# Kernel optimization log

Hardware: AMD Instinct MI355X
Metric: run time of the kernel (lower is better)

The kernel has to match this reference:

```python
import jax, jax.numpy as jnp
import numpy as np

EPS = 1e-5  # BatchNorm eps (torch default)


def setup_inputs() -> dict:
    key = jax.random.key(0)
    ks = jax.random.split(key, 12)
    C, Ci, B, H, W = 64, 32, 2, 96, 96  # plane, inter_plane=plane//2

    def n(k, shape, s=0.05):
        return jax.random.normal(k, shape, jnp.float32) * s

    return {
        "xA": jax.random.normal(ks[0], (B, C, H, W), jnp.float32),
        "xB": jax.random.normal(ks[1], (B, C, H, W), jnp.float32),
        "Wk": n(ks[2], (Ci, C)), "bk": n(ks[3], (Ci,)),
        "Wv": n(ks[4], (Ci, C)), "bv": n(ks[5], (Ci,)),
        "Wq": n(ks[6], (Ci, C)), "bq": n(ks[7], (Ci,)),
        "Wg": n(ks[8], (Ci, Ci)),  # conv_wg, 1x1 Conv1d, no bias
        "g1_gamma": jnp.ones((Ci,), jnp.float32), "g1_beta": jnp.zeros((Ci,), jnp.float32),
        "g1_mean": jnp.zeros((Ci,), jnp.float32), "g1_var": jnp.ones((Ci,), jnp.float32),
        "Wo": n(ks[9], (C, Ci)), "bo": n(ks[10], (C,)),
        "g2_gamma": jnp.ones((C,), jnp.float32), "g2_beta": jnp.zeros((C,), jnp.float32),
        "g2_mean": jnp.zeros((C,), jnp.float32), "g2_var": jnp.ones((C,), jnp.float32),
    }


def reference(xA, xB, Wk, bk, Wv, bv, Wq, bq, Wg,
              g1_gamma, g1_beta, g1_mean, g1_var,
              Wo, bo, g2_gamma, g2_beta, g2_mean, g2_var):
    B, C, H, W = xB.shape
    N = H * W
    # 1x1 conv2d projections -> [B, Ci, N]
    k = (jnp.einsum('bchw,oc->bohw', xA, Wk) + bk[None, :, None, None]).reshape(B, -1, N)
    v = (jnp.einsum('bchw,oc->bohw', xA, Wv) + bv[None, :, None, None]).reshape(B, -1, N)
    q = (jnp.einsum('bchw,oc->bohw', xB, Wq) + bq[None, :, None, None]).reshape(B, -1, N)
    # AV = softmax(v^T @ q, axis=2)  -> [B, N, N]
    A = jax.nn.softmax(jnp.einsum('bcn,bcm->bnm', v, q), axis=2)
    # k @ AV -> [B, Ci, N]
    av = jnp.einsum('bcn,bnm->bcm', k, A)
    # conv_wg (1x1 conv1d, no bias) + BatchNorm1d (inference form)
    av = jnp.einsum('oc,bcn->bon', Wg, av)
    av = (av - g1_mean[None, :, None]) * (g1_gamma / jnp.sqrt(g1_var + EPS))[None, :, None] + g1_beta[None, :, None]
    av = av.reshape(B, -1, H, W)
    # out: 1x1 conv2d -> plane, BatchNorm2d, residual, relu
    o = jnp.einsum('oc,bchw->bohw', Wo, av) + bo[None, :, None, None]
    o = (o - g2_mean[None, :, None, None]) * (g2_gamma / jnp.sqrt(g2_var + EPS))[None, :, None, None] + g2_beta[None, :, None, None]
    return jax.nn.relu(o + xB)
```

## Files before the change

### kernel.cpp

```cpp
#include <hip/hip_runtime.h>
#include <hip/hip_bf16.h>

#define CI 32
#define CC 64
#define NBATCH 2
#define NPIX 9216
#define NSD 24
#define LOG2E 1.4426950408889634f

typedef __attribute__((ext_vector_type(8))) short s16x8;
typedef __attribute__((ext_vector_type(4))) short s16x4;
typedef __attribute__((ext_vector_type(4))) float f32x4;
typedef __attribute__((ext_vector_type(2))) unsigned int u32x2;
typedef __attribute__((ext_vector_type(4))) unsigned int u32x4;

static __device__ __forceinline__ unsigned cvtpk(float a, float b) {
    unsigned d;
    asm("v_cvt_pk_bf16_f32 %0, %1, %2" : "=v"(d) : "v"(a), "v"(b));
    return d;
}
static __device__ __forceinline__ short f2b(float f) {
    union { float f; unsigned u; } v; v.f = f;
    return (short)((v.u + 0x7FFFu + ((v.u >> 16) & 1u)) >> 16);
}
static __device__ __forceinline__ float b2f(short s) {
    union { unsigned u; float f; } v; v.u = ((unsigned)(unsigned short)s) << 16;
    return v.f;
}

__global__ __launch_bounds__(256) void k_proj(
    const float* __restrict__ xA, const float* __restrict__ xB,
    const float* __restrict__ Wk, const float* __restrict__ bk,
    const float* __restrict__ Wv, const float* __restrict__ bv,
    const float* __restrict__ Wq, const float* __restrict__ bq,
    short* __restrict__ vT, short* __restrict__ qT, short* __restrict__ kC)
{
    int mode = blockIdx.y;
    const float* W    = mode == 0 ? Wk : (mode == 1 ? Wv : Wq);
    const float* bias = mode == 0 ? bk : (mode == 1 ? bv : bq);
    const float* X    = mode == 2 ? xB : xA;

    __shared__ float sW[CI * CC];
    __shared__ float sb[CI];
    __shared__ float spart[3][64][33];
    for (int i = threadIdx.x; i < CI * CC; i += 256) sW[i] = W[i];
    if (threadIdx.x < CI) sb[threadIdx.x] = bias[threadIdx.x];
    __syncthreads();

    int q4 = threadIdx.x >> 6;
    int lp = threadIdx.x & 63;
    int idx = blockIdx.x * 64 + lp;
    int b = idx / NPIX, n = idx % NPIX;

    float acc[CI];
    #pragma unroll
    for (int o = 0; o < CI; o++) acc[o] = 0.f;

    const float* px = X + (size_t)b * CC * NPIX + n;
    #pragma unroll
    for (int cc = 0; cc < 16; cc++) {
        int c = q4 * 16 + cc;
        float x = px[(size_t)c * NPIX];
        #pragma unroll
        for (int o = 0; o < CI; o++) acc[o] += sW[o * CC + c] * x;
    }
    if (q4) {
        #pragma unroll
        for (int o = 0; o < CI; o++) spart[q4 - 1][lp][o] = acc[o];
    }
    __syncthreads();
    if (q4 == 0) {
        #pragma unroll
        for (int o = 0; o < CI; o++)
            acc[o] += spart[0][lp][o] + spart[1][lp][o] + spart[2][lp][o] + sb[o];
        if (mode == 0) {
            #pragma unroll
            for (int o = 0; o < CI; o++)
                kC[((size_t)b * CI + o) * NPIX + n] = f2b(acc[o]);
        } else {
            float sc = (mode == 2) ? LOG2E : 1.0f;
            short* dst = (mode == 1 ? vT : qT) + ((size_t)b * NPIX + n) * CI;
            #pragma unroll
            for (int v4 = 0; v4 < 4; v4++) {
                u32x4 pk;
                #pragma unroll
                for (int j = 0; j < 4; j++)
                    pk[j] = cvtpk(acc[v4 * 8 + 2 * j] * sc, acc[v4 * 8 + 2 * j + 1] * sc);
                ((u32x4*)dst)[v4] = pk;
            }
        }
    }
}

__global__ __launch_bounds__(128) void k_denom(
    const short* __restrict__ vT, const short* __restrict__ qT,
    float* __restrict__ sum_part)
{
    int w = threadIdx.x >> 6, lane = threadIdx.x & 63;
    int r = lane & 15, g = lane >> 4;
    int b = blockIdx.y;
    int nb = blockIdx.x * 64 + w * 32;

    const short* vb = vT + (size_t)b * NPIX * CI;
    s16x8 a0 = *(const s16x8*)(vb + (size_t)(nb + r) * CI + 8 * g);
    s16x8 a1 = *(const s16x8*)(vb + (size_t)(nb + 16 + r) * CI + 8 * g);

    f32x4 s0 = {0.f, 0.f, 0.f, 0.f}, s1 = {0.f, 0.f, 0.f, 0.f};
    f32x4 s0b = {0.f, 0.f, 0.f, 0.f}, s1b = {0.f, 0.f, 0.f, 0.f};
    f32x4 z  = {0.f, 0.f, 0.f, 0.f};
    const short* qb = qT + (size_t)b * NPIX * CI;
    int mlo = blockIdx.z * (NPIX / NSD);
    int mhi = mlo + NPIX / NSD;
    for (int m0 = mlo; m0 < mhi; m0 += 64) {
        s16x8 q0 = *(const s16x8*)(qb + (size_t)(m0 + r) * CI + 8 * g);
        s16x8 q1 = *(const s16x8*)(qb + (size_t)(m0 + 16 + r) * CI + 8 * g);
        s16x8 q2 = *(const s16x8*)(qb + (size_t)(m0 + 32 + r) * CI + 8 * g);
        s16x8 q3 = *(const s16x8*)(qb + (size_t)(m0 + 48 + r) * CI + 8 * g);
        f32x4 t00 = __builtin_amdgcn_mfma_f32_16x16x32_bf16(a0, q0, z, 0, 0, 0);
        f32x4 t01 = __builtin_amdgcn_mfma_f32_16x16x32_bf16(a0, q1, z, 0, 0, 0);
        f32x4 t10 = __builtin_amdgcn_mfma_f32_16x16x32_bf16(a1, q0, z, 0, 0, 0);
        f32x4 t11 = __builtin_amdgcn_mfma_f32_16x16x32_bf16(a1, q1, z, 0, 0, 0);
        f32x4 u00 = __builtin_amdgcn_mfma_f32_16x16x32_bf16(a0, q2, z, 0, 0, 0);
        f32x4 u01 = __builtin_amdgcn_mfma_f32_16x16x32_bf16(a0, q3, z, 0, 0, 0);
        f32x4 u10 = __builtin_amdgcn_mfma_f32_16x16x32_bf16(a1, q2, z, 0, 0, 0);
        f32x4 u11 = __builtin_amdgcn_mfma_f32_16x16x32_bf16(a1, q3, z, 0, 0, 0);
        #pragma unroll
        for (int e = 0; e < 4; e++) {
            s0[e]  += __builtin_amdgcn_exp2f(t00[e]) + __builtin_amdgcn_exp2f(t01[e]);
            s1[e]  += __builtin_amdgcn_exp2f(t10[e]) + __builtin_amdgcn_exp2f(t11[e]);
            s0b[e] += __builtin_amdgcn_exp2f(u00[e]) + __builtin_amdgcn_exp2f(u01[e]);
            s1b[e] += __builtin_amdgcn_exp2f(u10[e]) + __builtin_amdgcn_exp2f(u11[e]);
        }
    }
    #pragma unroll
    for (int e = 0; e < 4; e++) { s0[e] += s0b[e]; s1[e] += s1b[e]; }
    #pragma unroll
    for (int mask = 1; mask < 16; mask <<= 1) {
        #pragma unroll
        for (int e = 0; e < 4; e++) {
            s0[e] += __shfl_xor(s0[e], mask, 64);
            s1[e] += __shfl_xor(s1[e], mask, 64);
        }
    }
    if (r == 0) {
        float* sp = sum_part + ((size_t)blockIdx.z * NBATCH + b) * NPIX;
        #pragma unroll
        for (int e = 0; e < 4; e++) {
            sp[nb + 4 * g + e]      = s0[e];
            sp[nb + 16 + 4 * g + e] = s1[e];
        }
    }
}

__global__ __launch_bounds__(256) void k_invd(
    const float* __restrict__ sum_part, float* __restrict__ invd)
{
    int idx = blockIdx.x * 256 + threadIdx.x;
    float s = 0.f;
    #pragma unroll
    for (int zz = 0; zz < NSD; zz++)
        s += sum_part[(size_t)zz * NBATCH * NPIX + idx];
    invd[idx] = 1.0f / s;
}

__global__ __launch_bounds__(256) void k_scale(
    short* __restrict__ kC, const float* __restrict__ invd)
{
    int idx = blockIdx.x * 256 + threadIdx.x;
    int n = idx % NPIX;
    int b = idx / (CI * NPIX);
    kC[idx] = f2b(b2f(kC[idx]) * invd[b * NPIX + n]);
}

__global__ __launch_bounds__(128) void k_attn(
    const short* __restrict__ vT, const short* __restrict__ qT,
    const short* __restrict__ kC, short* __restrict__ avp, int slice)
{
    __shared__ short plds[2][2][32][36];
    int w = threadIdx.x >> 6, lane = threadIdx.x & 63;
    int r = lane & 15, g = lane >> 4;
    int b = blockIdx.y;
    int m0 = blockIdx.x * 64 + w * 32;

    const short* qb = qT + (size_t)b * NPIX * CI;
    s16x8 qb0 = *(const s16x8*)(qb + (size_t)(m0 + r) * CI + 8 * g);
    s16x8 qb1 = *(const s16x8*)(qb + (size_t)(m0 + 16 + r) * CI + 8 * g);

    const short* vb = vT + (size_t)b * NPIX * CI;
    const short* k0 = kC + ((size_t)b * CI + r) * NPIX;
    const short* k1 = k0 + (size_t)16 * NPIX;

    f32x4 acc00 = {0,0,0,0}, acc01 = {0,0,0,0}, acc10 = {0,0,0,0}, acc11 = {0,0,0,0};
    f32x4 z = {0,0,0,0};

    int nlo = blockIdx.z * slice;
    int nhi = nlo + slice;
    for (int n0 = nlo; n0 < nhi; n0 += 64) {
        #pragma unroll
        for (int par = 0; par < 2; par++) {
            int nn = n0 + par * 32;
            s16x8 a0  = *(const s16x8*)(vb + (size_t)(nn + r) * CI + 8 * g);
            s16x8 a1  = *(const s16x8*)(vb + (size_t)(nn + 16 + r) * CI + 8 * g);
            s16x8 ka0 = *(const s16x8*)(k0 + nn + 8 * g);
            s16x8 ka1 = *(const s16x8*)(k1 + nn + 8 * g);

            f32x4 t00 = __builtin_amdgcn_mfma_f32_16x16x32_bf16(a0, qb0, z, 0, 0, 0);
            f32x4 t01 = __builtin_amdgcn_mfma_f32_16x16x32_bf16(a0, qb1, z, 0, 0, 0);
            f32x4 t10 = __builtin_amdgcn_mfma_f32_16x16x32_bf16(a1, qb0, z, 0, 0, 0);
            f32x4 t11 = __builtin_amdgcn_mfma_f32_16x16x32_bf16(a1, qb1, z, 0, 0, 0);

            u32x2 w00 = {cvtpk(__builtin_amdgcn_exp2f(t00[0]), __builtin_amdgcn_exp2f(t00[1])),
                         cvtpk(__builtin_amdgcn_exp2f(t00[2]), __builtin_amdgcn_exp2f(t00[3]))};
            u32x2 w10 = {cvtpk(__builtin_amdgcn_exp2f(t10[0]), __builtin_amdgcn_exp2f(t10[1])),
                         cvtpk(__builtin_amdgcn_exp2f(t10[2]), __builtin_amdgcn_exp2f(t10[3]))};
            u32x2 w01 = {cvtpk(__builtin_amdgcn_exp2f(t01[0]), __builtin_amdgcn_exp2f(t01[1])),
                         cvtpk(__builtin_amdgcn_exp2f(t01[2]), __builtin_amdgcn_exp2f(t01[3]))};
            u32x2 w11 = {cvtpk(__builtin_amdgcn_exp2f(t11[0]), __builtin_amdgcn_exp2f(t11[1])),
                         cvtpk(__builtin_amdgcn_exp2f(t11[2]), __builtin_amdgcn_exp2f(t11[3]))};

            *(u32x2*)&plds[w][par][r][4 * g]           = w00;
            *(u32x2*)&plds[w][par][r][16 + 4 * g]      = w10;
            *(u32x2*)&plds[w][par][16 + r][4 * g]      = w01;
            *(u32x2*)&plds[w][par][16 + r][16 + 4 * g] = w11;

            s16x4 l0 = *(const s16x4*)&plds[w][par][r][8 * g];
            s16x4 h0 = *(const s16x4*)&plds[w][par][r][8 * g + 4];
            s16x4 l1 = *(const s16x4*)&plds[w][par][16 + r][8 * g];
            s16x4 h1 = *(const s16x4*)&plds[w][par][16 + r][8 * g + 4];
            s16x8 pb0 = {l0[0], l0[1], l0[2], l0[3], h0[0], h0[1], h0[2], h0[3]};
            s16x8 pb1 = {l1[0], l1[1], l1[2], l1[3], h1[0], h1[1], h1[2], h1[3]};

            acc00 = __builtin_amdgcn_mfma_f32_16x16x32_bf16(ka0, pb0, acc00, 0, 0, 0);
            acc10 = __builtin_amdgcn_mfma_f32_16x16x32_bf16(ka1, pb0, acc10, 0, 0, 0);
            acc01 = __builtin_amdgcn_mfma_f32_16x16x32_bf16(ka0, pb1, acc01, 0, 0, 0);
            acc11 = __builtin_amdgcn_mfma_f32_16x16x32_bf16(ka1, pb1, acc11, 0, 0, 0);
        }
    }

    short* dst = avp + ((size_t)blockIdx.z * NBATCH + b) * NPIX * CI;
    u32x2 o00 = {cvtpk(acc00[0], acc00[1]), cvtpk(acc00[2], acc00[3])};
    u32x2 o10 = {cvtpk(acc10[0], acc10[1]), cvtpk(acc10[2], acc10[3])};
    u32x2 o01 = {cvtpk(acc01[0], acc01[1]), cvtpk(acc01[2], acc01[3])};
    u32x2 o11 = {cvtpk(acc11[0], acc11[1]), cvtpk(acc11[2], acc11[3])};
    *(u32x2*)(dst + (size_t)(m0 + r) * CI + 4 * g)           = o00;
    *(u32x2*)(dst + (size_t)(m0 + r) * CI + 16 + 4 * g)      = o10;
    *(u32x2*)(dst + (size_t)(m0 + 16 + r) * CI + 4 * g)      = o01;
    *(u32x2*)(dst + (size_t)(m0 + 16 + r) * CI + 16 + 4 * g) = o11;
}

__global__ __launch_bounds__(256) void e_red(
    const short* __restrict__ avp, short* __restrict__ av, int nsa)
{
    int idx = blockIdx.x * 256 + threadIdx.x;
    const unsigned* src = (const unsigned*)avp;
    float lo = 0.f, hi = 0.f;
    for (int zz = 0; zz < nsa; zz++) {
        unsigned p = src[(size_t)zz * (NBATCH * NPIX * CI / 2) + idx];
        lo += b2f((short)(p & 0xFFFF));
        hi += b2f((short)(p >> 16));
    }
    ((unsigned*)av)[idx] = cvtpk(lo, hi);
}

__global__ __launch_bounds__(256) void e_fused(
    const short* __restrict__ av,
    const float* __restrict__ Wg,
    const float* __restrict__ g1g, const float* __restrict__ g1b,
    const float* __restrict__ g1m, const float* __restrict__ g1v,
    const float* __restrict__ Wo, const float* __restrict__ bo,
    const float* __restrict__ g2g, const float* __restrict__ g2b,
    const float* __restrict__ g2m, const float* __restrict__ g2v,
    const float* __restrict__ xB, float* __restrict__ out)
{
    __shared__ float sWg[CI * CI], sWo[16 * CI], s1[CI], t1[CI], s2[16], t2[16];
    int t = threadIdx.x, jq = blockIdx.y;
    for (int i = t; i < CI * CI; i += 256) sWg[i] = Wg[i];
    for (int i = t; i < 16 * CI; i += 256) sWo[i] = Wo[jq * 16 * CI + i];
    if (t < CI) {
        float s = g1g[t] * rsqrtf(g1v[t] + 1e-5f);
        s1[t] = s; t1[t] = g1b[t] - g1m[t] * s;
    } else if (t < CI + 16) {
        int j = jq * 16 + (t - CI);
        float s = g2g[j] * rsqrtf(g2v[j] + 1e-5f);
        s2[t - CI] = s; t2[t - CI] = g2b[j] - g2m[j] * s + bo[j] * s;
    }
    __syncthreads();

    int idx = blockIdx.x * 256 + t;
    int b = idx / NPIX, m = idx % NPIX;

    float a[CI];
    const short* p = av + (size_t)idx * CI;
    #pragma unroll
    for (int v8 = 0; v8 < 4; v8++) {
        s16x8 tv = *(const s16x8*)(p + 8 * v8);
        #pragma unroll
        for (int j = 0; j < 8; j++) a[8 * v8 + j] = b2f(tv[j]);
    }
    float a2[CI];
    #pragma unroll
    for (int o = 0; o < CI; o++) {
        float acc = 0.f;
        #pragma unroll
        for (int c = 0; c < CI; c++) acc += sWg[o * CI + c] * a[c];
        a2[o] = acc * s1[o] + t1[o];
    }
    #pragma unroll
    for (int jj = 0; jj < 16; jj++) {
        float acc = 0.f;
        #pragma unroll
        for (int o = 0; o < CI; o++) acc += sWo[jj * CI + o] * a2[o];
        acc = acc * s2[jj] + t2[jj];
        size_t oi = ((size_t)b * CC + jq * 16 + jj) * NPIX + m;
        float res = acc + xB[oi];
        out[oi] = res > 0.f ? res : 0.f;
    }
}

extern "C" void kernel_launch(void* const* d_in, const int* in_sizes, int n_in,
                              void* d_out, int out_size, void* d_ws, size_t ws_size,
                              hipStream_t stream)
{
    const float* xA = (const float*)d_in[0];
    const float* xB = (const float*)d_in[1];
    const float* Wk = (const float*)d_in[2];
    const float* bk = (const float*)d_in[3];
    const float* Wv = (const float*)d_in[4];
    const float* bv = (const float*)d_in[5];
    const float* Wq = (const float*)d_in[6];
    const float* bq = (const float*)d_in[7];
    const float* Wg = (const float*)d_in[8];
    const float* g1g = (const float*)d_in[9];
    const float* g1b = (const float*)d_in[10];
    const float* g1m = (const float*)d_in[11];
    const float* g1v = (const float*)d_in[12];
    const float* Wo = (const float*)d_in[13];
    const float* bo = (const float*)d_in[14];
    const float* g2g = (const float*)d_in[15];
    const float* g2b = (const float*)d_in[16];
    const float* g2m = (const float*)d_in[17];
    const float* g2v = (const float*)d_in[18];
    float* out = (float*)d_out;

    char* ws = (char*)d_ws;
    const size_t SZB = (size_t)NBATCH * NPIX * CI * 2;
    short* vT = (short*)(ws);
    short* qT = (short*)(ws + SZB);
    short* kC = (short*)(ws + 2 * SZB);
    float* invd = (float*)(ws + 3 * SZB);
    char*  region = ws + 3 * SZB + (size_t)NBATCH * NPIX * 4;
    float* sum_part = (float*)region;
    short* avp = (short*)region;
    short* av = vT;

    const size_t base = 3 * SZB + (size_t)NBATCH * NPIX * 4;
    int nsa = (ws_size >= base + (size_t)16 * NBATCH * NPIX * CI * 2) ? 16 : 8;
    int slice = NPIX / nsa;

    k_proj<<<dim3(NBATCH * NPIX / 64, 3), dim3(256), 0, stream>>>(
        xA, xB, Wk, bk, Wv, bv, Wq, bq, vT, qT, kC);
    k_denom<<<dim3(NPIX / 64, NBATCH, NSD), dim3(128), 0, stream>>>(
        vT, qT, sum_part);
    k_invd<<<dim3(NBATCH * NPIX / 256), dim3(256), 0, stream>>>(
        sum_part, invd);
    k_scale<<<dim3(NBATCH * CI * NPIX / 256), dim3(256), 0, stream>>>(
        kC, invd);
    k_attn<<<dim3(NPIX / 64, NBATCH, nsa), dim3(128), 0, stream>>>(
        vT, qT, kC, avp, slice);
    e_red<<<dim3(NBATCH * NPIX * CI / 2 / 256), dim3(256), 0, stream>>>(
        avp, av, nsa);
    e_fused<<<dim3(NBATCH * NPIX / 256, 4), dim3(256), 0, stream>>>(
        av, Wg, g1g, g1b, g1m, g1v, Wo, bo, g2g, g2b, g2m, g2v, xB, out);
}
```

Before: 133.5 us.

## Software-prefetch operands in attention kernels and move epilogue convs onto MFMA

The denominator and attention kernels now run one wave per block and prefetch the next iteration's V, Q and K fragments into registers before doing the current MFMAs, so global load latency is hidden by compute. The attention LDS staging buffer shrinks to one wave's tile. The epilogue replaces the scalar per-pixel 32x32 and 32x64 FMA loops with bf16 MFMAs, folding the BatchNorm scales into the weights, and computes all 64 output channels in one block instead of four. This cuts epilogue ALU work but adds bf16 rounding of the intermediate activations and weights, and the smaller blocks give the scheduler less to overlap within each CU.

```diff
diff --git a/kernel.cpp b/kernel.cpp
--- a/kernel.cpp
+++ b/kernel.cpp
@@ -26,6 +26,9 @@
 static __device__ __forceinline__ float b2f(short s) {
     union { unsigned u; float f; } v; v.u = ((unsigned)(unsigned short)s) << 16;
     return v.f;
+}
+static __device__ __forceinline__ s16x8 asS16x8(u32x4 v) {
+    union { u32x4 u; s16x8 s; } c; c.u = v; return c.s;
 }
 
 __global__ __launch_bounds__(256) void k_proj(
@@ -92,48 +95,43 @@
     }
 }
 
-__global__ __launch_bounds__(128) void k_denom(
+__global__ __launch_bounds__(64) void k_denom(
     const short* __restrict__ vT, const short* __restrict__ qT,
     float* __restrict__ sum_part)
 {
-    int w = threadIdx.x >> 6, lane = threadIdx.x & 63;
+    int lane = threadIdx.x;
     int r = lane & 15, g = lane >> 4;
     int b = blockIdx.y;
-    int nb = blockIdx.x * 64 + w * 32;
+    int nb = blockIdx.x * 32;
 
     const short* vb = vT + (size_t)b * NPIX * CI;
     s16x8 a0 = *(const s16x8*)(vb + (size_t)(nb + r) * CI + 8 * g);
     s16x8 a1 = *(const s16x8*)(vb + (size_t)(nb + 16 + r) * CI + 8 * g);
 
     f32x4 s0 = {0.f, 0.f, 0.f, 0.f}, s1 = {0.f, 0.f, 0.f, 0.f};
-    f32x4 s0b = {0.f, 0.f, 0.f, 0.f}, s1b = {0.f, 0.f, 0.f, 0.f};
     f32x4 z  = {0.f, 0.f, 0.f, 0.f};
     const short* qb = qT + (size_t)b * NPIX * CI;
     int mlo = blockIdx.z * (NPIX / NSD);
     int mhi = mlo + NPIX / NSD;
-    for (int m0 = mlo; m0 < mhi; m0 += 64) {
-        s16x8 q0 = *(const s16x8*)(qb + (size_t)(m0 + r) * CI + 8 * g);
-        s16x8 q1 = *(const s16x8*)(qb + (size_t)(m0 + 16 + r) * CI + 8 * g);
-        s16x8 q2 = *(const s16x8*)(qb + (size_t)(m0 + 32 + r) * CI + 8 * g);
-        s16x8 q3 = *(const s16x8*)(qb + (size_t)(m0 + 48 + r) * CI + 8 * g);
+
+    s16x8 q0 = *(const s16x8*)(qb + (size_t)(mlo + r) * CI + 8 * g);
+    s16x8 q1 = *(const s16x8*)(qb + (size_t)(mlo + 16 + r) * CI + 8 * g);
+    for (int m0 = mlo; m0 < mhi; m0 += 32) {
+        int np = (m0 + 32 < mhi) ? m0 + 32 : mlo;
+        s16x8 nq0 = *(const s16x8*)(qb + (size_t)(np + r) * CI + 8 * g);
+        s16x8 nq1 = *(const s16x8*)(qb + (size_t)(np + 16 + r) * CI + 8 * g);
+
         f32x4 t00 = __builtin_amdgcn_mfma_f32_16x16x32_bf16(a0, q0, z, 0, 0, 0);
         f32x4 t01 = __builtin_amdgcn_mfma_f32_16x16x32_bf16(a0, q1, z, 0, 0, 0);
         f32x4 t10 = __builtin_amdgcn_mfma_f32_16x16x32_bf16(a1, q0, z, 0, 0, 0);
         f32x4 t11 = __builtin_amdgcn_mfma_f32_16x16x32_bf16(a1, q1, z, 0, 0, 0);
-        f32x4 u00 = __builtin_amdgcn_mfma_f32_16x16x32_bf16(a0, q2, z, 0, 0, 0);
-        f32x4 u01 = __builtin_amdgcn_mfma_f32_16x16x32_bf16(a0, q3, z, 0, 0, 0);
-        f32x4 u10 = __builtin_amdgcn_mfma_f32_16x16x32_bf16(a1, q2, z, 0, 0, 0);
-        f32x4 u11 = __builtin_amdgcn_mfma_f32_16x16x32_bf16(a1, q3, z, 0, 0, 0);
         #pragma unroll
         for (int e = 0; e < 4; e++) {
-            s0[e]  += __builtin_amdgcn_exp2f(t00[e]) + __builtin_amdgcn_exp2f(t01[e]);
-            s1[e]  += __builtin_amdgcn_exp2f(t10[e]) + __builtin_amdgcn_exp2f(t11[e]);
-            s0b[e] += __builtin_amdgcn_exp2f(u00[e]) + __builtin_amdgcn_exp2f(u01[e]);
-            s1b[e] += __builtin_amdgcn_exp2f(u10[e]) + __builtin_amdgcn_exp2f(u11[e]);
-        }
-    }
-    #pragma unroll
-    for (int e = 0; e < 4; e++) { s0[e] += s0b[e]; s1[e] += s1b[e]; }
+            s0[e] += __builtin_amdgcn_exp2f(t00[e]) + __builtin_amdgcn_exp2f(t01[e]);
+            s1[e] += __builtin_amdgcn_exp2f(t10[e]) + __builtin_amdgcn_exp2f(t11[e]);
+        }
+        q0 = nq0; q1 = nq1;
+    }
     #pragma unroll
     for (int mask = 1; mask < 16; mask <<= 1) {
         #pragma unroll
@@ -172,15 +170,15 @@
     kC[idx] = f2b(b2f(kC[idx]) * invd[b * NPIX + n]);
 }
 
-__global__ __launch_bounds__(128) void k_attn(
+__global__ __launch_bounds__(64) void k_attn(
     const short* __restrict__ vT, const short* __restrict__ qT,
     const short* __restrict__ kC, short* __restrict__ avp, int slice)
 {
-    __shared__ short plds[2][2][32][36];
-    int w = threadIdx.x >> 6, lane = threadIdx.x & 63;
+    __shared__ short plds[32][36];
+    int lane = threadIdx.x;
     int r = lane & 15, g = lane >> 4;
     int b = blockIdx.y;
-    int m0 = blockIdx.x * 64 + w * 32;
+    int m0 = blockIdx.x * 32;
 
     const short* qb = qT + (size_t)b * NPIX * CI;
     s16x8 qb0 = *(const s16x8*)(qb + (size_t)(m0 + r) * CI + 8 * g);
@@ -195,46 +193,51 @@
 
     int nlo = blockIdx.z * slice;
     int nhi = nlo + slice;
-    for (int n0 = nlo; n0 < nhi; n0 += 64) {
-        #pragma unroll
-        for (int par = 0; par < 2; par++) {
-            int nn = n0 + par * 32;
-            s16x8 a0  = *(const s16x8*)(vb + (size_t)(nn + r) * CI + 8 * g);
-            s16x8 a1  = *(const s16x8*)(vb + (size_t)(nn + 16 + r) * CI + 8 * g);
-            s16x8 ka0 = *(const s16x8*)(k0 + nn + 8 * g);
-            s16x8 ka1 = *(const s16x8*)(k1 + nn + 8 * g);
-
-            f32x4 t00 = __builtin_amdgcn_mfma_f32_16x16x32_bf16(a0, qb0, z, 0, 0, 0);
-            f32x4 t01 = __builtin_amdgcn_mfma_f32_16x16x32_bf16(a0, qb1, z, 0, 0, 0);
-            f32x4 t10 = __builtin_amdgcn_mfma_f32_16x16x32_bf16(a1, qb0, z, 0, 0, 0);
-            f32x4 t11 = __builtin_amdgcn_mfma_f32_16x16x32_bf16(a1, qb1, z, 0, 0, 0);
-
-            u32x2 w00 = {cvtpk(__builtin_amdgcn_exp2f(t00[0]), __builtin_amdgcn_exp2f(t00[1])),
-                         cvtpk(__builtin_amdgcn_exp2f(t00[2]), __builtin_amdgcn_exp2f(t00[3]))};
-            u32x2 w10 = {cvtpk(__builtin_amdgcn_exp2f(t10[0]), __builtin_amdgcn_exp2f(t10[1])),
-                         cvtpk(__builtin_amdgcn_exp2f(t10[2]), __builtin_amdgcn_exp2f(t10[3]))};
-            u32x2 w01 = {cvtpk(__builtin_amdgcn_exp2f(t01[0]), __builtin_amdgcn_exp2f(t01[1])),
-                         cvtpk(__builtin_amdgcn_exp2f(t01[2]), __builtin_amdgcn_exp2f(t01[3]))};
-            u32x2 w11 = {cvtpk(__builtin_amdgcn_exp2f(t11[0]), __builtin_amdgcn_exp2f(t11[1])),
-                         cvtpk(__builtin_amdgcn_exp2f(t11[2]), __builtin_amdgcn_exp2f(t11[3]))};
-
-            *(u32x2*)&plds[w][par][r][4 * g]           = w00;
-            *(u32x2*)&plds[w][par][r][16 + 4 * g]      = w10;
-            *(u32x2*)&plds[w][par][16 + r][4 * g]      = w01;
-            *(u32x2*)&plds[w][par][16 + r][16 + 4 * g] = w11;
-
-            s16x4 l0 = *(const s16x4*)&plds[w][par][r][8 * g];
-            s16x4 h0 = *(const s16x4*)&plds[w][par][r][8 * g + 4];
-            s16x4 l1 = *(const s16x4*)&plds[w][par][16 + r][8 * g];
-            s16x4 h1 = *(const s16x4*)&plds[w][par][16 + r][8 * g + 4];
-            s16x8 pb0 = {l0[0], l0[1], l0[2], l0[3], h0[0], h0[1], h0[2], h0[3]};
-            s16x8 pb1 = {l1[0], l1[1], l1[2], l1[3], h1[0], h1[1], h1[2], h1[3]};
-
-            acc00 = __builtin_amdgcn_mfma_f32_16x16x32_bf16(ka0, pb0, acc00, 0, 0, 0);
-            acc10 = __builtin_amdgcn_mfma_f32_16x16x32_bf16(ka1, pb0, acc10, 0, 0, 0);
-            acc01 = __builtin_amdgcn_mfma_f32_16x16x32_bf16(ka0, pb1, acc01, 0, 0, 0);
-            acc11 = __builtin_amdgcn_mfma_f32_16x16x32_bf16(ka1, pb1, acc11, 0, 0, 0);
-        }
+
+    s16x8 a0  = *(const s16x8*)(vb + (size_t)(nlo + r) * CI + 8 * g);
+    s16x8 a1  = *(const s16x8*)(vb + (size_t)(nlo + 16 + r) * CI + 8 * g);
+    s16x8 ka0 = *(const s16x8*)(k0 + nlo + 8 * g);
+    s16x8 ka1 = *(const s16x8*)(k1 + nlo + 8 * g);
+
+    for (int n0 = nlo; n0 < nhi; n0 += 32) {
+        int np = (n0 + 32 < nhi) ? n0 + 32 : nlo;
+        s16x8 na0  = *(const s16x8*)(vb + (size_t)(np + r) * CI + 8 * g);
+        s16x8 na1  = *(const s16x8*)(vb + (size_t)(np + 16 + r) * CI + 8 * g);
+        s16x8 nka0 = *(const s16x8*)(k0 + np + 8 * g);
+        s16x8 nka1 = *(const s16x8*)(k1 + np + 8 * g);
+
+        f32x4 t00 = __builtin_amdgcn_mfma_f32_16x16x32_bf16(a0, qb0, z, 0, 0, 0);
+        f32x4 t01 = __builtin_amdgcn_mfma_f32_16x16x32_bf16(a0, qb1, z, 0, 0, 0);
+        f32x4 t10 = __builtin_amdgcn_mfma_f32_16x16x32_bf16(a1, qb0, z, 0, 0, 0);
+        f32x4 t11 = __builtin_amdgcn_mfma_f32_16x16x32_bf16(a1, qb1, z, 0, 0, 0);
+
+        u32x2 w00 = {cvtpk(__builtin_amdgcn_exp2f(t00[0]), __builtin_amdgcn_exp2f(t00[1])),
+                     cvtpk(__builtin_amdgcn_exp2f(t00[2]), __builtin_amdgcn_exp2f(t00[3]))};
+        u32x2 w10 = {cvtpk(__builtin_amdgcn_exp2f(t10[0]), __builtin_amdgcn_exp2f(t10[1])),
+                     cvtpk(__builtin_amdgcn_exp2f(t10[2]), __builtin_amdgcn_exp2f(t10[3]))};
+        u32x2 w01 = {cvtpk(__builtin_amdgcn_exp2f(t01[0]), __builtin_amdgcn_exp2f(t01[1])),
+                     cvtpk(__builtin_amdgcn_exp2f(t01[2]), __builtin_amdgcn_exp2f(t01[3]))};
+        u32x2 w11 = {cvtpk(__builtin_amdgcn_exp2f(t11[0]), __builtin_amdgcn_exp2f(t11[1])),
+                     cvtpk(__builtin_amdgcn_exp2f(t11[2]), __builtin_amdgcn_exp2f(t11[3]))};
+
+        *(u32x2*)&plds[r][4 * g]           = w00;
+        *(u32x2*)&plds[r][16 + 4 * g]      = w10;
+        *(u32x2*)&plds[16 + r][4 * g]      = w01;
+        *(u32x2*)&plds[16 + r][16 + 4 * g] = w11;
+
+        s16x4 l0 = *(const s16x4*)&plds[r][8 * g];
+        s16x4 h0 = *(const s16x4*)&plds[r][8 * g + 4];
+        s16x4 l1 = *(const s16x4*)&plds[16 + r][8 * g];
+        s16x4 h1 = *(const s16x4*)&plds[16 + r][8 * g + 4];
+        s16x8 pb0 = {l0[0], l0[1], l0[2], l0[3], h0[0], h0[1], h0[2], h0[3]};
+        s16x8 pb1 = {l1[0], l1[1], l1[2], l1[3], h1[0], h1[1], h1[2], h1[3]};
+
+        acc00 = __builtin_amdgcn_mfma_f32_16x16x32_bf16(ka0, pb0, acc00, 0, 0, 0);
+        acc10 = __builtin_amdgcn_mfma_f32_16x16x32_bf16(ka1, pb0, acc10, 0, 0, 0);
+        acc01 = __builtin_amdgcn_mfma_f32_16x16x32_bf16(ka0, pb1, acc01, 0, 0, 0);
+        acc11 = __builtin_amdgcn_mfma_f32_16x16x32_bf16(ka1, pb1, acc11, 0, 0, 0);
+
+        a0 = na0; a1 = na1; ka0 = nka0; ka1 = nka1;
     }
 
     short* dst = avp + ((size_t)blockIdx.z * NBATCH + b) * NPIX * CI;
@@ -272,48 +275,69 @@
     const float* __restrict__ g2m, const float* __restrict__ g2v,
     const float* __restrict__ xB, float* __restrict__ out)
 {
-    __shared__ float sWg[CI * CI], sWo[16 * CI], s1[CI], t1[CI], s2[16], t2[16];
-    int t = threadIdx.x, jq = blockIdx.y;
-    for (int i = t; i < CI * CI; i += 256) sWg[i] = Wg[i];
-    for (int i = t; i < 16 * CI; i += 256) sWo[i] = Wo[jq * 16 * CI + i];
-    if (t < CI) {
-        float s = g1g[t] * rsqrtf(g1v[t] + 1e-5f);
-        s1[t] = s; t1[t] = g1b[t] - g1m[t] * s;
-    } else if (t < CI + 16) {
-        int j = jq * 16 + (t - CI);
-        float s = g2g[j] * rsqrtf(g2v[j] + 1e-5f);
-        s2[t - CI] = s; t2[t - CI] = g2b[j] - g2m[j] * s + bo[j] * s;
+    __shared__ float s1s[CI], t1s[CI], s2s[CC], t2s[CC];
+    __shared__ short sa2[4][16][36];
+    int t = threadIdx.x;
+    if (t < CC) {
+        float s = g2g[t] * rsqrtf(g2v[t] + 1e-5f);
+        s2s[t] = s; t2s[t] = g2b[t] - g2m[t] * s + bo[t] * s;
+    } else if (t < CC + CI) {
+        int o = t - CC;
+        float s = g1g[o] * rsqrtf(g1v[o] + 1e-5f);
+        s1s[o] = s; t1s[o] = g1b[o] - g1m[o] * s;
     }
     __syncthreads();
 
-    int idx = blockIdx.x * 256 + t;
-    int b = idx / NPIX, m = idx % NPIX;
-
-    float a[CI];
-    const short* p = av + (size_t)idx * CI;
-    #pragma unroll
-    for (int v8 = 0; v8 < 4; v8++) {
-        s16x8 tv = *(const s16x8*)(p + 8 * v8);
-        #pragma unroll
-        for (int j = 0; j < 8; j++) a[8 * v8 + j] = b2f(tv[j]);
-    }
-    float a2[CI];
-    #pragma unroll
-    for (int o = 0; o < CI; o++) {
-        float acc = 0.f;
-        #pragma unroll
-        for (int c = 0; c < CI; c++) acc += sWg[o * CI + c] * a[c];
-        a2[o] = acc * s1[o] + t1[o];
-    }
-    #pragma unroll
-    for (int jj = 0; jj < 16; jj++) {
-        float acc = 0.f;
-        #pragma unroll
-        for (int o = 0; o < CI; o++) acc += sWo[jj * CI + o] * a2[o];
-        acc = acc * s2[jj] + t2[jj];
-        size_t oi = ((size_t)b * CC + jq * 16 + jj) * NPIX + m;
-        float res = acc + xB[oi];
-        out[oi] = res > 0.f ? res : 0.f;
+    int w = t >> 6, lane = t & 63;
+    int r = lane & 15, g = lane >> 4;
+    int idx0 = blockIdx.x * 64 + w * 16;
+    int b = idx0 / NPIX;
+    int mcol = (idx0 % NPIX) + r;
+
+    const float* wg0 = Wg + r * CI + 8 * g;
+    const float* wg1 = Wg + (16 + r) * CI + 8 * g;
+    float sA = s1s[r], sB = s1s[16 + r];
+    u32x4 a1l, a1h;
+    #pragma unroll
+    for (int j = 0; j < 4; j++) {
+        a1l[j] = cvtpk(wg0[2 * j] * sA, wg0[2 * j + 1] * sA);
+        a1h[j] = cvtpk(wg1[2 * j] * sB, wg1[2 * j + 1] * sB);
+    }
+    s16x8 A1lo = asS16x8(a1l), A1hi = asS16x8(a1h);
+
+    s16x8 Bav = *(const s16x8*)(av + (size_t)(idx0 + r) * CI + 8 * g);
+
+    f32x4 z = {0, 0, 0, 0};
+    f32x4 d1lo = __builtin_amdgcn_mfma_f32_16x16x32_bf16(A1lo, Bav, z, 0, 0, 0);
+    f32x4 d1hi = __builtin_amdgcn_mfma_f32_16x16x32_bf16(A1hi, Bav, z, 0, 0, 0);
+
+    u32x2 plo = {cvtpk(d1lo[0] + t1s[4 * g],     d1lo[1] + t1s[4 * g + 1]),
+                 cvtpk(d1lo[2] + t1s[4 * g + 2], d1lo[3] + t1s[4 * g + 3])};
+    u32x2 phi = {cvtpk(d1hi[0] + t1s[16 + 4 * g],     d1hi[1] + t1s[16 + 4 * g + 1]),
+                 cvtpk(d1hi[2] + t1s[16 + 4 * g + 2], d1hi[3] + t1s[16 + 4 * g + 3])};
+    *(u32x2*)&sa2[w][r][4 * g]      = plo;
+    *(u32x2*)&sa2[w][r][16 + 4 * g] = phi;
+
+    s16x4 l0 = *(const s16x4*)&sa2[w][r][8 * g];
+    s16x4 h0 = *(const s16x4*)&sa2[w][r][8 * g + 4];
+    s16x8 B2 = {l0[0], l0[1], l0[2], l0[3], h0[0], h0[1], h0[2], h0[3]};
+
+    #pragma unroll
+    for (int h = 0; h < 4; h++) {
+        const float* wo = Wo + (size_t)(16 * h + r) * CI + 8 * g;
+        float s = s2s[16 * h + r];
+        u32x4 aw;
+        #pragma unroll
+        for (int j = 0; j < 4; j++)
+            aw[j] = cvtpk(wo[2 * j] * s, wo[2 * j + 1] * s);
+        f32x4 d2 = __builtin_amdgcn_mfma_f32_16x16x32_bf16(asS16x8(aw), B2, z, 0, 0, 0);
+        #pragma unroll
+        for (int e = 0; e < 4; e++) {
+            int ch = 16 * h + 4 * g + e;
+            size_t oi = ((size_t)b * CC + ch) * NPIX + mcol;
+            float v = d2[e] + t2s[ch] + xB[oi];
+            out[oi] = v > 0.f ? v : 0.f;
+        }
     }
 }
 
@@ -359,16 +383,16 @@
 
     k_proj<<<dim3(NBATCH * NPIX / 64, 3), dim3(256), 0, stream>>>(
         xA, xB, Wk, bk, Wv, bv, Wq, bq, vT, qT, kC);
-    k_denom<<<dim3(NPIX / 64, NBATCH, NSD), dim3(128), 0, stream>>>(
+    k_denom<<<dim3(NPIX / 32, NBATCH, NSD), dim3(64), 0, stream>>>(
         vT, qT, sum_part);
     k_invd<<<dim3(NBATCH * NPIX / 256), dim3(256), 0, stream>>>(
         sum_part, invd);
     k_scale<<<dim3(NBATCH * CI * NPIX / 256), dim3(256), 0, stream>>>(
         kC, invd);
-    k_attn<<<dim3(NPIX / 64, NBATCH, nsa), dim3(128), 0, stream>>>(
+    k_attn<<<dim3(NPIX / 32, NBATCH, nsa), dim3(64), 0, stream>>>(
         vT, qT, kC, avp, slice);
     e_red<<<dim3(NBATCH * NPIX * CI / 2 / 256), dim3(256), 0, stream>>>(
         avp, av, nsa);
-    e_fused<<<dim3(NBATCH * NPIX / 256, 4), dim3(256), 0, stream>>>(
+    e_fused<<<dim3(NBATCH * NPIX / 64), dim3(256), 0, stream>>>(
         av, Wg, g1g, g1b, g1m, g1v, Wo, bo, g2g, g2b, g2m, g2v, xB, out);
 }
```

Result: faster. 127.0 us (-4.8%).
